# Performance work log

Measured on AMD Instinct MI355X. Metric: run time of the kernel, lower is better.

Reference implementation:

```python
import jax, jax.numpy as jnp
import numpy as np
import math

HEADS = 8
DIM_HEAD = 64


def setup_inputs() -> dict:
    key = jax.random.key(0)
    k1, k2, k3 = jax.random.split(key, 3)
    b, n, dim = 4, 2048, 512
    inner = HEADS * DIM_HEAD  # 512
    x = jax.random.normal(k1, (b, n, dim), dtype=jnp.float32)
    W_qkv = jax.random.normal(k2, (dim, 4 * inner), dtype=jnp.float32) * (dim ** -0.5)
    W_out = jax.random.normal(k3, (2 * inner, dim), dtype=jnp.float32) * ((2 * inner) ** -0.5)
    b_out = jnp.zeros((dim,), dtype=jnp.float32)
    return {"x": x, "W_qkv": W_qkv, "W_out": W_out, "b_out": b_out}


def reference(x, W_qkv, W_out, b_out):
    b, n, d = x.shape
    h, dh = HEADS, DIM_HEAD
    scale = dh ** -0.5
    qkvt = x @ W_qkv  # [b, n, 4*h*dh]
    q, k, v, t = jnp.split(qkvt, 4, axis=-1)
    # 'b n (h d) -> b h n d'
    def to_heads(z):
        return z.reshape(b, n, h, dh).transpose(0, 2, 1, 3)
    q, k, v, t = map(to_heads, (q, k, v, t))

    # Branch 1: standard softmax attention
    dots = jnp.einsum('bhid,bhjd->bhij', q, k) * scale
    attn1 = jax.nn.softmax(dots, axis=-1)
    out1 = jnp.einsum('bhij,bhjd->bhid', attn1, v)

    # Branch 2: fixed positional-decay attention (shared across b, h; no repeat needed)
    pos = jnp.arange(1, n + 1, dtype=x.dtype)  # linspace(1, n, n)
    tg = jnp.abs(pos[None, :] - pos[:, None])  # |j - i|, [n, n]
    attn2 = jnp.exp(-tg / jnp.asarray(math.e, dtype=x.dtype))
    # NOTE: original divides by sum(-1) WITHOUT keepdim -> broadcasts over columns:
    # attn2[i, j] / sum_k attn2[j, k]
    attn2 = attn2 / attn2.sum(-1)
    out2 = jnp.einsum('ij,bhjd->bhid', attn2, t)

    out = jnp.concatenate([out1, out2], axis=-1)  # [b, h, n, 2*dh]
    out = out.transpose(0, 2, 1, 3).reshape(b, n, 2 * h * dh)  # 'b h n d -> b n (h d)'
    return out @ W_out + b_out
```

## Files before the change

### kernel.cpp

```cpp
#include <hip/hip_runtime.h>
#include <hip/hip_bf16.h>

#define B_ 4
#define N_ 2048
#define D_ 512
#define H_ 8
#define DH_ 64

typedef float float4_ __attribute__((ext_vector_type(4)));
typedef int int2_ __attribute__((ext_vector_type(2)));
typedef int int4_ __attribute__((ext_vector_type(4)));
typedef unsigned short ushort4_ __attribute__((ext_vector_type(4)));
typedef unsigned short ushort8_ __attribute__((ext_vector_type(8)));
typedef __bf16 bf16x8 __attribute__((ext_vector_type(8)));
typedef _Float16 half2_ __attribute__((ext_vector_type(2)));
typedef _Float16 half4_ __attribute__((ext_vector_type(4)));
typedef _Float16 half8_ __attribute__((ext_vector_type(8)));

#if __has_builtin(__builtin_amdgcn_exp2f)
#define EXP2(x) __builtin_amdgcn_exp2f(x)
#else
#define EXP2(x) exp2f(x)
#endif

__device__ __forceinline__ float b2f(unsigned short u) {
  union { unsigned int u; float f; } v; v.u = ((unsigned int)u) << 16; return v.f;
}
__device__ __forceinline__ unsigned short f2b(float f) {
  union { float f; unsigned int u; } v; v.f = f;
  unsigned int r = v.u + 0x7fffu + ((v.u >> 16) & 1u);
  return (unsigned short)(r >> 16);
}
__device__ __forceinline__ half4_ pk4(float a, float b, float c, float d) {
  half2_ lo = __builtin_bit_cast(half2_, __builtin_amdgcn_cvt_pkrtz(a, b));
  half2_ hi = __builtin_bit_cast(half2_, __builtin_amdgcn_cvt_pkrtz(c, d));
  return __builtin_bit_cast(half4_,
      (int2_){__builtin_bit_cast(int, lo), __builtin_bit_cast(int, hi)});
}

#define GLD16(gp, lp)                                                        \
  __builtin_amdgcn_global_load_lds(                                          \
      (const __attribute__((address_space(1))) unsigned int*)(gp),           \
      (__attribute__((address_space(3))) unsigned int*)(lp), 16, 0, 0)

__device__ __forceinline__ bool detect_fp32_local(
    const unsigned short* __restrict__ xhdr, int* cnt_sh) {
  if (threadIdx.x == 0) *cnt_sh = 0;
  __syncthreads();
  unsigned int e = (xhdr[threadIdx.x] >> 7) & 0xFFu;
  if (e >= 134u) atomicAdd(cnt_sh, 1);
  __syncthreads();
  return *cnt_sh > 16;
}

__device__ __forceinline__ void transpose_conv(
    const void* __restrict__ src, unsigned short* __restrict__ dst,
    int R, int C, int bx, int by, bool ofp) {
  __shared__ unsigned short tile[32][33];
  const int c0 = bx * 32, r0 = by * 32;
  const int tx = threadIdx.x & 31, ty = threadIdx.x >> 5;
#pragma unroll
  for (int k = 0; k < 4; ++k) {
    int r = ty + k * 8;
    long idx = (long)(r0 + r) * C + c0 + tx;
    tile[r][tx] = ofp ? f2b(((const float*)src)[idx])
                      : ((const unsigned short*)src)[idx];
  }
  __syncthreads();
#pragma unroll
  for (int k = 0; k < 4; ++k) {
    int c = ty + k * 8;
    dst[(long)(c0 + c) * R + r0 + tx] = tile[tx][c];
  }
}

__global__ __launch_bounds__(256) void prep_all(
    const void* __restrict__ xraw, const void* __restrict__ Wqraw,
    const void* __restrict__ Woraw, unsigned short* __restrict__ xb,
    unsigned short* __restrict__ WqT, unsigned short* __restrict__ WoT,
    unsigned short* __restrict__ Wband) {
  __shared__ int cnt_sh;
  const bool ofp = detect_fp32_local((const unsigned short*)xraw, &cnt_sh);
  const int bid = blockIdx.x;
  if (bid < 4096) {
    int i4 = bid * 256 + threadIdx.x;
    ushort4_ o;
    if (ofp) {
      float4_ v = ((const float4_*)xraw)[i4];
      o[0] = f2b(v[0]); o[1] = f2b(v[1]); o[2] = f2b(v[2]); o[3] = f2b(v[3]);
    } else {
      o = ((const ushort4_*)xraw)[i4];
    }
    *(ushort4_*)(xb + (long)i4 * 4) = o;
  } else if (bid < 5120) {
    const int b2 = bid - 4096;
    transpose_conv(Wqraw, WqT, 512, 2048, b2 % 64, b2 / 64, ofp);
  } else if (bid < 5632) {
    const int b2 = bid - 5120;
    transpose_conv(Woraw, WoT, 1024, 512, b2 % 16, b2 / 16, ofp);
  } else {
    constexpr float INV_E = 0.36787944117144233f;
    constexpr float R1 = 0.69220062755534635f;
    constexpr float INV_1MR = 3.2488706f;
    const int i = bid - 5632;
    const int krel = threadIdx.x;
    const int j = (i >> 6) * 64 - 96 + krel;
    float c = 0.f;
    if (j >= 0 && j < N_) {
      float wgt = __expf(-fabsf((float)(i - j)) * INV_E);
      float rj = __expf(-(float)j * INV_E);
      float rnj = __expf(-(float)(N_ - 1 - j) * INV_E);
      float S = 1.f + R1 * (2.f - rj - rnj) * INV_1MR;
      c = wgt / S;
    }
    _Float16 hv = (_Float16)c;
    Wband[i * 256 + krel] = __builtin_bit_cast(unsigned short, hv);
  }
}

#define MFMA16x32(d, a, b) \
  d = __builtin_amdgcn_mfma_f32_16x16x32_bf16(a, b, d, 0, 0, 0)

__global__ __launch_bounds__(512, 2) void gemm256(
    const unsigned short* __restrict__ A, const unsigned short* __restrict__ Bt,
    unsigned short* __restrict__ C, int M, int N, int K) {
  __shared__ unsigned short As[2][16384];
  __shared__ unsigned short Bs[2][16384];
  const int tid = threadIdx.x;
  const int w = tid >> 6, lane = tid & 63, l16 = lane & 15, quad = lane >> 4;
  const int wm = w >> 2, wn = w & 3;
  const long tm = (long)blockIdx.x * 256, tn = (long)blockIdx.y * 256;

  const int srow = tid >> 3;
  const int sch = (tid & 7) ^ (srow & 7);
  const unsigned short* gA = A + (tm + srow) * (long)K + sch * 8;
  const unsigned short* gB = Bt + (tn + srow) * (long)K + sch * 8;

  const int xr8 = l16 & 7;
  const int ch0 = ((0 + quad) ^ xr8) * 8;
  const int ch1 = ((4 + quad) ^ xr8) * 8;
  const int rowA0 = (wm * 128 + l16) * 64;
  const int rowB0 = (wn * 64 + l16) * 64;

  float4_ acc[8][4] = {};

  auto stage = [&](int t, int bufn) __attribute__((always_inline)) {
#pragma unroll
    for (int r = 0; r < 4; ++r)
      GLD16(gA + (long)(r * 64) * K + t * 64, &As[bufn][r * 4096 + w * 512]);
#pragma unroll
    for (int r = 0; r < 4; ++r)
      GLD16(gB + (long)(r * 64) * K + t * 64, &Bs[bufn][r * 4096 + w * 512]);
  };

  stage(0, 0);
  asm volatile("s_waitcnt vmcnt(0)" ::: "memory");
  __builtin_amdgcn_s_barrier();

  const int NT = K >> 6;
  for (int t = 0; t < NT; ++t) {
    const int buf = t & 1;
    const unsigned short* as = As[buf];
    const unsigned short* bs = Bs[buf];
    bf16x8 af[8], bq[4], br[4];
#pragma unroll
    for (int mi = 0; mi < 4; ++mi) {
      af[mi * 2]     = __builtin_bit_cast(bf16x8, *(const int4_*)&as[rowA0 + mi * 1024 + ch0]);
      af[mi * 2 + 1] = __builtin_bit_cast(bf16x8, *(const int4_*)&as[rowA0 + mi * 1024 + ch1]);
    }
#pragma unroll
    for (int ni = 0; ni < 2; ++ni) {
      bq[ni * 2]     = __builtin_bit_cast(bf16x8, *(const int4_*)&bs[rowB0 + ni * 1024 + ch0]);
      bq[ni * 2 + 1] = __builtin_bit_cast(bf16x8, *(const int4_*)&bs[rowB0 + ni * 1024 + ch1]);
    }
    if (t + 1 < NT) stage(t + 1, buf ^ 1);
    __builtin_amdgcn_s_barrier();
    asm volatile("s_waitcnt lgkmcnt(0)" ::: "memory");
    __builtin_amdgcn_sched_barrier(0);
    __builtin_amdgcn_s_setprio(1);
#pragma unroll
    for (int mi = 0; mi < 4; ++mi)
#pragma unroll
      for (int ni = 0; ni < 2; ++ni) {
        MFMA16x32(acc[mi][ni], af[mi * 2], bq[ni * 2]);
        MFMA16x32(acc[mi][ni], af[mi * 2 + 1], bq[ni * 2 + 1]);
      }
    __builtin_amdgcn_s_setprio(0);
    __builtin_amdgcn_s_barrier();
#pragma unroll
    for (int ni = 0; ni < 2; ++ni) {
      br[ni * 2]     = __builtin_bit_cast(bf16x8, *(const int4_*)&bs[rowB0 + (2 + ni) * 1024 + ch0]);
      br[ni * 2 + 1] = __builtin_bit_cast(bf16x8, *(const int4_*)&bs[rowB0 + (2 + ni) * 1024 + ch1]);
    }
    __builtin_amdgcn_s_barrier();
    asm volatile("s_waitcnt lgkmcnt(0)" ::: "memory");
    __builtin_amdgcn_sched_barrier(0);
    __builtin_amdgcn_s_setprio(1);
#pragma unroll
    for (int mi = 0; mi < 4; ++mi)
#pragma unroll
      for (int ni = 0; ni < 2; ++ni) {
        MFMA16x32(acc[mi][2 + ni], af[mi * 2], br[ni * 2]);
        MFMA16x32(acc[mi][2 + ni], af[mi * 2 + 1], br[ni * 2 + 1]);
      }
    __builtin_amdgcn_s_setprio(0);
    __builtin_amdgcn_s_barrier();
#pragma unroll
    for (int mi = 0; mi < 4; ++mi) {
      af[mi * 2]     = __builtin_bit_cast(bf16x8, *(const int4_*)&as[rowA0 + (4 + mi) * 1024 + ch0]);
      af[mi * 2 + 1] = __builtin_bit_cast(bf16x8, *(const int4_*)&as[rowA0 + (4 + mi) * 1024 + ch1]);
    }
    __builtin_amdgcn_s_barrier();
    asm volatile("s_waitcnt lgkmcnt(0)" ::: "memory");
    __builtin_amdgcn_sched_barrier(0);
    __builtin_amdgcn_s_setprio(1);
#pragma unroll
    for (int mi = 0; mi < 4; ++mi)
#pragma unroll
      for (int ni = 0; ni < 2; ++ni) {
        MFMA16x32(acc[4 + mi][2 + ni], af[mi * 2], br[ni * 2]);
        MFMA16x32(acc[4 + mi][2 + ni], af[mi * 2 + 1], br[ni * 2 + 1]);
      }
    __builtin_amdgcn_s_setprio(0);
    __builtin_amdgcn_s_barrier();
#pragma unroll
    for (int ni = 0; ni < 2; ++ni) {
      bq[ni * 2]     = __builtin_bit_cast(bf16x8, *(const int4_*)&bs[rowB0 + ni * 1024 + ch0]);
      bq[ni * 2 + 1] = __builtin_bit_cast(bf16x8, *(const int4_*)&bs[rowB0 + ni * 1024 + ch1]);
    }
    __builtin_amdgcn_s_barrier();
    asm volatile("s_waitcnt lgkmcnt(0)" ::: "memory");
    __builtin_amdgcn_sched_barrier(0);
    __builtin_amdgcn_s_setprio(1);
#pragma unroll
    for (int mi = 0; mi < 4; ++mi)
#pragma unroll
      for (int ni = 0; ni < 2; ++ni) {
        MFMA16x32(acc[4 + mi][ni], af[mi * 2], bq[ni * 2]);
        MFMA16x32(acc[4 + mi][ni], af[mi * 2 + 1], bq[ni * 2 + 1]);
      }
    __builtin_amdgcn_s_setprio(0);
    asm volatile("s_waitcnt vmcnt(0)" ::: "memory");
    __builtin_amdgcn_sched_barrier(0);
    __builtin_amdgcn_s_barrier();
  }
#pragma unroll
  for (int ni = 0; ni < 4; ++ni) {
    long col = tn + wn * 64 + ni * 16 + l16;
#pragma unroll
    for (int mi = 0; mi < 8; ++mi)
#pragma unroll
      for (int r = 0; r < 4; ++r) {
        long row = tm + wm * 128 + mi * 16 + quad * 4 + r;
        C[row * N + col] = f2b(acc[mi][ni][r]);
      }
  }
}

__global__ __launch_bounds__(512, 2) void gemm_o(
    const unsigned short* __restrict__ A, const unsigned short* __restrict__ Bt,
    void* __restrict__ C, const void* __restrict__ bias_raw,
    const unsigned short* __restrict__ xhdr) {
  __shared__ int cnt_sh;
  const bool ofp = detect_fp32_local(xhdr, &cnt_sh);
  __shared__ unsigned short As[2][8192];
  __shared__ unsigned short Bs[2][8192];
  constexpr int K = 1024, N = 512;
  const int tid = threadIdx.x;
  const int w = tid >> 6, lane = tid & 63, l16 = lane & 15, quad = lane >> 4;
  const int wm = w >> 2, wn = w & 3;
  const long tm = (long)blockIdx.x * 128, tn = (long)blockIdx.y * 128;
  const int srow = tid >> 3;
  const int sch = (tid & 7) ^ (srow & 7);
  const unsigned short* gA = A + (tm + srow) * (long)K + sch * 8;
  const unsigned short* gB = Bt + (tn + srow) * (long)K + sch * 8;
  const int xr8 = l16 & 7;
  const int ch0 = ((0 + quad) ^ xr8) * 8;
  const int ch1 = ((4 + quad) ^ xr8) * 8;
  const int rowA0 = (wm * 64 + l16) * 64;
  const int rowB0 = (wn * 32 + l16) * 64;
  float4_ acc[4][2] = {};

  auto stage = [&](int t, int bufn) __attribute__((always_inline)) {
#pragma unroll
    for (int r = 0; r < 2; ++r)
      GLD16(gA + (long)(r * 64) * K + t * 64, &As[bufn][r * 4096 + w * 512]);
#pragma unroll
    for (int r = 0; r < 2; ++r)
      GLD16(gB + (long)(r * 64) * K + t * 64, &Bs[bufn][r * 4096 + w * 512]);
  };

  stage(0, 0);
  asm volatile("s_waitcnt vmcnt(0)" ::: "memory");
  __builtin_amdgcn_s_barrier();

  const int NT = K >> 6;
  for (int t = 0; t < NT; ++t) {
    const int buf = t & 1;
    const unsigned short* as = As[buf];
    const unsigned short* bs = Bs[buf];
    bf16x8 af[8], bf0[2], bf1[2];
#pragma unroll
    for (int mi = 0; mi < 4; ++mi) {
      af[mi * 2]     = __builtin_bit_cast(bf16x8, *(const int4_*)&as[rowA0 + mi * 1024 + ch0]);
      af[mi * 2 + 1] = __builtin_bit_cast(bf16x8, *(const int4_*)&as[rowA0 + mi * 1024 + ch1]);
    }
    bf0[0] = __builtin_bit_cast(bf16x8, *(const int4_*)&bs[rowB0 + ch0]);
    bf0[1] = __builtin_bit_cast(bf16x8, *(const int4_*)&bs[rowB0 + ch1]);
    if (t + 1 < NT) stage(t + 1, buf ^ 1);
    __builtin_amdgcn_s_barrier();
    asm volatile("s_waitcnt lgkmcnt(0)" ::: "memory");
    __builtin_amdgcn_sched_barrier(0);
    __builtin_amdgcn_s_setprio(1);
#pragma unroll
    for (int mi = 0; mi < 4; ++mi) {
      MFMA16x32(acc[mi][0], af[mi * 2], bf0[0]);
      MFMA16x32(acc[mi][0], af[mi * 2 + 1], bf0[1]);
    }
    __builtin_amdgcn_s_setprio(0);
    __builtin_amdgcn_s_barrier();
    bf1[0] = __builtin_bit_cast(bf16x8, *(const int4_*)&bs[rowB0 + 1024 + ch0]);
    bf1[1] = __builtin_bit_cast(bf16x8, *(const int4_*)&bs[rowB0 + 1024 + ch1]);
    __builtin_amdgcn_s_barrier();
    asm volatile("s_waitcnt lgkmcnt(0)" ::: "memory");
    __builtin_amdgcn_sched_barrier(0);
    __builtin_amdgcn_s_setprio(1);
#pragma unroll
    for (int mi = 0; mi < 4; ++mi) {
      MFMA16x32(acc[mi][1], af[mi * 2], bf1[0]);
      MFMA16x32(acc[mi][1], af[mi * 2 + 1], bf1[1]);
    }
    __builtin_amdgcn_s_setprio(0);
    asm volatile("s_waitcnt vmcnt(0)" ::: "memory");
    __builtin_amdgcn_sched_barrier(0);
    __builtin_amdgcn_s_barrier();
  }
#pragma unroll
  for (int nb = 0; nb < 2; ++nb) {
    long col = tn + wn * 32 + nb * 16 + l16;
    float bv = ofp ? ((const float*)bias_raw)[col]
                   : b2f(((const unsigned short*)bias_raw)[col]);
#pragma unroll
    for (int mb = 0; mb < 4; ++mb)
#pragma unroll
      for (int r = 0; r < 4; ++r) {
        long row = tm + wm * 64 + mb * 16 + quad * 4 + r;
        float val = acc[mb][nb][r] + bv;
        if (ofp) ((float*)C)[row * N + col] = val;
        else ((unsigned short*)C)[row * N + col] = f2b(val);
      }
  }
}

#define TSW 266
__global__ __launch_bounds__(256) void mid_all(
    const unsigned short* __restrict__ qkvt, unsigned short* __restrict__ Vt,
    const unsigned short* __restrict__ Wband, unsigned short* __restrict__ catb) {
  __shared__ __align__(16) unsigned short Ts[64 * TSW];
  const int bid = blockIdx.x;
  const int tid = threadIdx.x;
  if (bid < 512) {
    unsigned int* Td = (unsigned int*)Ts;
    const int bh = bid >> 4, b = bh >> 3, h = bh & 7;
    const int j0 = (bid & 15) * 128;
    const int dg = tid & 7;
#pragma unroll
    for (int it = 0; it < 2; ++it) {
      const int jp = (tid >> 3) + 32 * it;
      const long base =
          (long)(b * N_ + j0 + 2 * jp) * 2048 + 1024 + h * 64 + dg * 8;
      ushort8_ r0 = __builtin_bit_cast(ushort8_, *(const int4_*)&qkvt[base]);
      ushort8_ r1 = __builtin_bit_cast(ushort8_, *(const int4_*)&qkvt[base + 2048]);
#pragma unroll
      for (int e = 0; e < 8; ++e) {
        const int d = dg * 8 + e;
        const int S = (d >> 3) | ((d & 1) << 3);
        unsigned short h0 = __builtin_bit_cast(unsigned short, (_Float16)b2f(r0[e]));
        unsigned short h1 = __builtin_bit_cast(unsigned short, (_Float16)b2f(r1[e]));
        Td[d * 68 + (jp ^ (S << 2))] = (unsigned int)h0 | ((unsigned int)h1 << 16);
      }
    }
    __syncthreads();
#pragma unroll
    for (int it = 0; it < 4; ++it) {
      const int d = (tid >> 4) + 16 * it;
      const int ch = tid & 15;
      const int S = (d >> 3) | ((d & 1) << 3);
      int4_ v = *(const int4_*)&Td[d * 68 + ((ch ^ S) << 2)];
      *(int4_*)&Vt[((long)bh * 64 + d) * 2048 + j0 + ch * 8] = v;
    }
    return;
  }
  const int b2 = bid - 512;
  const int qtile = b2 & 31;
  const int bh = b2 >> 5, b = bh >> 3, h = bh & 7;
  const int jlo = qtile * 64 - 96;
  {
    unsigned int* Tsd = (unsigned int*)Ts;
    const int dg = tid & 7;
#pragma unroll
    for (int it = 0; it < 4; ++it) {
      const int kkp = (tid >> 3) + 32 * it;
      const int jA = jlo + 2 * kkp, jB = jA + 1;
      int4_ r0 = {}, r1 = {};
      if (jA >= 0 && jA < N_)
        r0 = *(const int4_*)&qkvt[(long)(b * N_ + jA) * 2048 + 1536 + h * 64 + dg * 8];
      if (jB >= 0 && jB < N_)
        r1 = *(const int4_*)&qkvt[(long)(b * N_ + jB) * 2048 + 1536 + h * 64 + dg * 8];
      ushort8_ u0 = __builtin_bit_cast(ushort8_, r0);
      ushort8_ u1 = __builtin_bit_cast(ushort8_, r1);
#pragma unroll
      for (int e = 0; e < 8; ++e) {
        const int d = dg * 8 + e;
        unsigned short h0 = __builtin_bit_cast(unsigned short, (_Float16)b2f(u0[e]));
        unsigned short h1 = __builtin_bit_cast(unsigned short, (_Float16)b2f(u1[e]));
        Tsd[d * 133 + kkp] = (unsigned int)h0 | ((unsigned int)h1 << 16);
      }
    }
  }
  __syncthreads();
  const int w = tid >> 6, lane = tid & 63, l16 = lane & 15, quad = lane >> 4;
  const int i_row = qtile * 64 + w * 16 + l16;
  const unsigned short* ap = Wband + i_row * 256;
  float4_ acc[4] = {};
#pragma unroll
  for (int kh = 0; kh < 8; ++kh) {
    half8_ af = __builtin_bit_cast(half8_, *(const int4_*)&ap[kh * 32 + quad * 8]);
#pragma unroll
    for (int nb = 0; nb < 4; ++nb) {
      half8_ bf = __builtin_bit_cast(half8_,
          *(const int4_*)&Ts[(nb * 16 + l16) * TSW + kh * 32 + quad * 8]);
      acc[nb] = __builtin_amdgcn_mfma_f32_16x16x32_f16(af, bf, acc[nb], 0, 0, 0);
    }
  }
#pragma unroll
  for (int nb = 0; nb < 4; ++nb)
#pragma unroll
    for (int r = 0; r < 4; ++r) {
      int row = qtile * 64 + w * 16 + quad * 4 + r;
      catb[(long)(b * N_ + row) * 1024 + h * 128 + 64 + nb * 16 + l16] =
          f2b(acc[nb][r]);
    }
}

__global__ __launch_bounds__(256) void flash_kernel(
    const unsigned short* __restrict__ qkvt, const unsigned short* __restrict__ Vt,
    unsigned short* __restrict__ catb) {
  __shared__ unsigned short Ks[2][64 * 64];
  __shared__ unsigned short Vs[2][64 * 64];
  const int flat = blockIdx.x + blockIdx.y * 16;
  const int slot = flat & 7, idx = flat >> 3;
  const int bh = slot * 4 + (idx >> 4);
  const int i0 = (idx & 15) * 128;
  const int b = bh >> 3, h = bh & 7;
  const int tid = threadIdx.x;
  const int w = tid >> 6, lane = tid & 63, l16 = lane & 15, quad = lane >> 4;
  const int srow8 = lane >> 3, sch = lane & 7;
  const int chK = sch ^ srow8;
  bf16x8 qf[2][2];
  {
    constexpr float SCL = 0.125f * 1.44269504088896f;
#pragma unroll
    for (int s2 = 0; s2 < 2; ++s2) {
      const long qrow =
          (long)(b * N_ + i0 + w * 32 + s2 * 16 + l16) * 2048 + h * 64;
#pragma unroll
      for (int kh = 0; kh < 2; ++kh) {
        ushort8_ raw = __builtin_bit_cast(ushort8_,
            *(const int4_*)&qkvt[qrow + kh * 32 + quad * 8]);
        ushort8_ sc;
#pragma unroll
        for (int e = 0; e < 8; ++e) sc[e] = f2b(b2f(raw[e]) * SCL);
        qf[s2][kh] = __builtin_bit_cast(bf16x8, sc);
      }
    }
  }
  const unsigned short* kp[2];
#pragma unroll
  for (int kh = 0; kh < 2; ++kh)
    kp[kh] = &Ks[0][l16 * 64 + (((kh * 4 + quad) ^ (l16 & 7)) * 8)];
  const unsigned short* vp[4];
#pragma unroll
  for (int c = 0; c < 4; ++c)
    vp[c] = &Vs[0][l16 * 64 + (((c * 2 + (quad >> 1)) ^ (l16 & 7)) * 8) +
                   (quad & 1) * 4];
  const unsigned short* kg[2];
  const unsigned short* vg[2];
#pragma unroll
  for (int g = 0; g < 2; ++g) {
    const int row = w * 16 + g * 8 + srow8;
    kg[g] = qkvt + (long)(b * N_ + row) * 2048 + 512 + h * 64 + chK * 8;
    vg[g] = Vt + ((long)bh * 64 + row) * 2048 + chK * 8;
  }
  float4_ O[2][4] = {};
  float4_ O5[2] = {};
  const half4_ ones = {(_Float16)1.f, (_Float16)1.f, (_Float16)1.f, (_Float16)1.f};

  auto stage_k = [&](int jt_, int buf_) __attribute__((always_inline)) {
    const int j0 = jt_ * 64;
#pragma unroll
    for (int g = 0; g < 2; ++g)
      GLD16(kg[g] + (long)j0 * 2048,
            (char*)&Ks[0][0] + buf_ * 8192 + (w * 16 + g * 8) * 128);
  };
  auto stage_v = [&](int jt_, int buf_) __attribute__((always_inline)) {
    const int j0 = jt_ * 64;
#pragma unroll
    for (int g = 0; g < 2; ++g)
      GLD16(vg[g] + j0,
            (char*)&Vs[0][0] + buf_ * 8192 + (w * 16 + g * 8) * 128);
  };
  auto pv_step = [&](half4_ (&pf)[2][4], int vb) __attribute__((always_inline)) {
#pragma unroll
    for (int c = 0; c < 4; ++c) {
#pragma unroll
      for (int dblk = 0; dblk < 4; ++dblk) {
        half4_ vfv = *(const half4_*)(vp[c] + vb + dblk * 1024);
#pragma unroll
        for (int s2 = 0; s2 < 2; ++s2)
          O[s2][dblk] = __builtin_amdgcn_mfma_f32_16x16x16f16(
              pf[s2][c], vfv, O[s2][dblk], 0, 0, 0);
      }
#pragma unroll
      for (int s2 = 0; s2 < 2; ++s2)
        O5[s2] = __builtin_amdgcn_mfma_f32_16x16x16f16(
            pf[s2][c], ones, O5[s2], 0, 0, 0);
    }
  };
  auto phase = [&](int i, half4_ (&pfp)[2][4], half4_ (&pfc)[2][4],
                   bool first, bool last) __attribute__((always_inline)) {
    if (!last) stage_k(i + 1, (i + 1) & 1);
    stage_v(i, i & 1);
    const int kb = (i & 1) * 4096;
    float4_ s[2][4] = {};
#pragma unroll
    for (int kh = 0; kh < 2; ++kh)
#pragma unroll
      for (int c = 0; c < 4; ++c) {
        bf16x8 kf = __builtin_bit_cast(bf16x8,
            *(const int4_*)(kp[kh] + kb + c * 1024));
#pragma unroll
        for (int s2 = 0; s2 < 2; ++s2)
          s[s2][c] = __builtin_amdgcn_mfma_f32_16x16x32_bf16(
              kf, qf[s2][kh], s[s2][c], 0, 0, 0);
      }
    if (!first) pv_step(pfp, ((i - 1) & 1) * 4096);
#pragma unroll
    for (int s2 = 0; s2 < 2; ++s2)
#pragma unroll
      for (int c = 0; c < 4; ++c)
        pfc[s2][c] = pk4(EXP2(s[s2][c][0]), EXP2(s[s2][c][1]),
                         EXP2(s[s2][c][2]), EXP2(s[s2][c][3]));
    __syncthreads();
  };

  half4_ pfA[2][4], pfB[2][4];
  stage_k(0, 0);
  asm volatile("s_waitcnt vmcnt(0)" ::: "memory");
  __builtin_amdgcn_s_barrier();
  phase(0, pfB, pfA, true, false);
  for (int jt = 1; jt < 31; jt += 2) {
    phase(jt, pfA, pfB, false, false);
    phase(jt + 1, pfB, pfA, false, false);
  }
  phase(31, pfA, pfB, false, true);
  pv_step(pfB, (31 & 1) * 4096);

#pragma unroll
  for (int s2 = 0; s2 < 2; ++s2) {
    float linv[4];
#pragma unroll
    for (int r = 0; r < 4; ++r) linv[r] = 1.f / O5[s2][r];
#pragma unroll
    for (int dblk = 0; dblk < 4; ++dblk)
#pragma unroll
      for (int r = 0; r < 4; ++r) {
        int row = i0 + w * 32 + s2 * 16 + quad * 4 + r;
        catb[(long)(b * N_ + row) * 1024 + h * 128 + dblk * 16 + l16] =
            f2b(O[s2][dblk][r] * linv[r]);
      }
  }
}

extern "C" void kernel_launch(void* const* d_in, const int* in_sizes, int n_in,
                              void* d_out, int out_size, void* d_ws, size_t ws_size,
                              hipStream_t stream) {
  char* ws = (char*)d_ws;
  unsigned short* qkvt = (unsigned short*)(ws);
  unsigned short* WqT  = (unsigned short*)(ws + (size_t)32 * 1024 * 1024);
  unsigned short* WoT  = (unsigned short*)(ws + (size_t)34 * 1024 * 1024);
  unsigned short* Vt   = (unsigned short*)(ws + (size_t)35 * 1024 * 1024);
  unsigned short* catb = (unsigned short*)(ws + (size_t)43 * 1024 * 1024);
  unsigned short* xb   = (unsigned short*)(ws + (size_t)59 * 1024 * 1024);
  unsigned short* Wband= (unsigned short*)(ws + (size_t)68 * 1024 * 1024);

  prep_all<<<7680, 256, 0, stream>>>(d_in[0], d_in[1], d_in[2],
                                     xb, WqT, WoT, Wband);
  gemm256<<<dim3(8192 / 256, 2048 / 256), 512, 0, stream>>>(
      xb, WqT, qkvt, 8192, 2048, 512);
  mid_all<<<1536, 256, 0, stream>>>(qkvt, Vt, Wband, catb);
  flash_kernel<<<dim3(2048 / 128, 32), 256, 0, stream>>>(qkvt, Vt, catb);
  gemm_o<<<dim3(8192 / 128, 512 / 128), 512, 0, stream>>>(
      catb, WoT, d_out, d_in[3], (const unsigned short*)d_in[0]);
}
```

Measured before the change: 183.5 us.

## Use 16x16x32 f16 MFMA for PV step with permuted K token staging

```diff
diff --git a/kernel.cpp b/kernel.cpp
--- a/kernel.cpp
+++ b/kernel.cpp
@@ -36,6 +36,11 @@
   half2_ hi = __builtin_bit_cast(half2_, __builtin_amdgcn_cvt_pkrtz(c, d));
   return __builtin_bit_cast(half4_,
       (int2_){__builtin_bit_cast(int, lo), __builtin_bit_cast(int, hi)});
+}
+__device__ __forceinline__ half8_ cat44(half4_ a, half4_ b) {
+  int2_ ia = __builtin_bit_cast(int2_, a), ib = __builtin_bit_cast(int2_, b);
+  int4_ r = {ia[0], ia[1], ib[0], ib[1]};
+  return __builtin_bit_cast(half8_, r);
 }
 
 #define GLD16(gp, lp)                                                        \
@@ -479,22 +484,24 @@
 #pragma unroll
   for (int kh = 0; kh < 2; ++kh)
     kp[kh] = &Ks[0][l16 * 64 + (((kh * 4 + quad) ^ (l16 & 7)) * 8)];
-  const unsigned short* vp[4];
-#pragma unroll
-  for (int c = 0; c < 4; ++c)
-    vp[c] = &Vs[0][l16 * 64 + (((c * 2 + (quad >> 1)) ^ (l16 & 7)) * 8) +
-                   (quad & 1) * 4];
+  const unsigned short* vp32[2];
+#pragma unroll
+  for (int wd = 0; wd < 2; ++wd)
+    vp32[wd] = &Vs[0][l16 * 64 + (((wd * 4 + quad) ^ (l16 & 7)) * 8)];
   const unsigned short* kg[2];
   const unsigned short* vg[2];
 #pragma unroll
   for (int g = 0; g < 2; ++g) {
-    const int row = w * 16 + g * 8 + srow8;
-    kg[g] = qkvt + (long)(b * N_ + row) * 2048 + 512 + h * 64 + chK * 8;
-    vg[g] = Vt + ((long)bh * 64 + row) * 2048 + chK * 8;
+    const int prow = w * 16 + g * 8 + srow8;
+    const int ptok = (prow & 0x20) | ((prow & 0x10) >> 2) |
+                     ((prow & 0x0C) << 1) | (prow & 3);
+    kg[g] = qkvt + (long)(b * N_ + ptok) * 2048 + 512 + h * 64 + chK * 8;
+    vg[g] = Vt + ((long)bh * 64 + prow) * 2048 + chK * 8;
   }
   float4_ O[2][4] = {};
   float4_ O5[2] = {};
-  const half4_ ones = {(_Float16)1.f, (_Float16)1.f, (_Float16)1.f, (_Float16)1.f};
+  const half8_ ones8 = {(_Float16)1.f, (_Float16)1.f, (_Float16)1.f, (_Float16)1.f,
+                        (_Float16)1.f, (_Float16)1.f, (_Float16)1.f, (_Float16)1.f};
 
   auto stage_k = [&](int jt_, int buf_) __attribute__((always_inline)) {
     const int j0 = jt_ * 64;
@@ -512,19 +519,19 @@
   };
   auto pv_step = [&](half4_ (&pf)[2][4], int vb) __attribute__((always_inline)) {
 #pragma unroll
-    for (int c = 0; c < 4; ++c) {
+    for (int wd = 0; wd < 2; ++wd) {
+      half8_ pa0 = cat44(pf[0][2 * wd], pf[0][2 * wd + 1]);
+      half8_ pa1 = cat44(pf[1][2 * wd], pf[1][2 * wd + 1]);
 #pragma unroll
       for (int dblk = 0; dblk < 4; ++dblk) {
-        half4_ vfv = *(const half4_*)(vp[c] + vb + dblk * 1024);
-#pragma unroll
-        for (int s2 = 0; s2 < 2; ++s2)
-          O[s2][dblk] = __builtin_amdgcn_mfma_f32_16x16x16f16(
-              pf[s2][c], vfv, O[s2][dblk], 0, 0, 0);
-      }
-#pragma unroll
-      for (int s2 = 0; s2 < 2; ++s2)
-        O5[s2] = __builtin_amdgcn_mfma_f32_16x16x16f16(
-            pf[s2][c], ones, O5[s2], 0, 0, 0);
+        half8_ vfv = *(const half8_*)(vp32[wd] + vb + dblk * 1024);
+        O[0][dblk] = __builtin_amdgcn_mfma_f32_16x16x32_f16(
+            pa0, vfv, O[0][dblk], 0, 0, 0);
+        O[1][dblk] = __builtin_amdgcn_mfma_f32_16x16x32_f16(
+            pa1, vfv, O[1][dblk], 0, 0, 0);
+      }
+      O5[0] = __builtin_amdgcn_mfma_f32_16x16x32_f16(pa0, ones8, O5[0], 0, 0, 0);
+      O5[1] = __builtin_amdgcn_mfma_f32_16x16x32_f16(pa1, ones8, O5[1], 0, 0, 0);
     }
   };
   auto phase = [&](int i, half4_ (&pfp)[2][4], half4_ (&pfc)[2][4],
```

After: 182.8 us. No clear change (-0.4%).
